# Kernel optimization log

Hardware: AMD Instinct MI355X
Metric: run time of the kernel (lower is better)

Reference implementation:

```python
import jax, jax.numpy as jnp
import numpy as np

N, E, IN, OUT, R, B = 50000, 800000, 16, 16, 90, 30


def setup_inputs() -> dict:
    key = jax.random.key(0)
    ks = jax.random.split(key, 9)
    h = jax.random.normal(ks[0], (N, IN), dtype=jnp.float32)
    he = jax.random.normal(ks[1], (E, IN), dtype=jnp.float32)
    Ws = jax.random.normal(ks[2], (OUT, IN), dtype=jnp.float32) * 0.1      # shared_weight.weight
    Wa = jax.random.normal(ks[3], (1, 3 * OUT), dtype=jnp.float32) * 0.1   # attn_fc.weight
    weight = jax.random.normal(ks[4], (B, IN, OUT), dtype=jnp.float32) * 0.1  # basis weights
    w_comp = jax.random.normal(ks[5], (R, B), dtype=jnp.float32) * 0.1        # basis coefficients
    src = jax.random.randint(ks[6], (E,), 0, N)
    dst = jax.random.randint(ks[7], (E,), 0, N)
    rel_type = jax.random.randint(ks[8], (E,), 0, R)
    return {"h": h, "he": he, "Ws": Ws, "Wa": Wa, "weight": weight,
            "w_comp": w_comp, "src": src, "dst": dst, "rel_type": rel_type}


def reference(h, he, Ws, Wa, weight, w_comp, src, dst, rel_type):
    n_nodes, in_dim = h.shape
    num_bases, _, out_dim = weight.shape
    num_rels = w_comp.shape[0]

    # Basis decomposition, replicating the original's reshape semantics exactly:
    # view [B,in,out] -> [in,B,out], matmul with w_comp [R,B] -> [in,R,out], view -> [R,in,out]
    V = weight.reshape(in_dim, num_bases, out_dim)
    W_rel = jnp.matmul(w_comp, V).reshape(num_rels, in_dim, out_dim)  # [R,in,out]

    # edge_attention: GAT-like score from concat(z_src, z_edge, z_dst)
    h_src = h[src]                      # [E,in]
    z_src = h_src @ Ws.T                # [E,out]
    z_dst = h[dst] @ Ws.T               # [E,out]
    z_e = he @ Ws.T                     # [E,out]
    e = jnp.concatenate([z_src, z_e, z_dst], axis=1) @ Wa.T  # [E,1] (no leaky_relu / no softmax in original)

    # message: per-edge relation-specific bmm, scaled by attention score
    msg = jnp.einsum('ei,eio->eo', h_src, W_rel[rel_type]) * e  # [E,out]

    # reduce: scatter-sum into destination nodes (bias=None, activation=None)
    h_out = jax.ops.segment_sum(msg, dst, num_segments=n_nodes)  # [N,out]
    return h_out
```

## Files before the change

### kernel.cpp

```cpp
#include <hip/hip_runtime.h>

#define N_NODES 50000
#define N_EDGES 800000
#define IN_DIM 16
#define OUT_DIM 16
#define N_RELS 90
#define N_BASES 30

#define CAP 64
#define LDS_STRIDE 260

#define PREP_BLOCKS 91
#define DOTS_BLOCKS 196
#define ZERO_BLOCKS 196
#define HZ_BLOCKS 782

#define NODES_PER_RBLK 256

__device__ __forceinline__ float4 shfl_xor4(float4 v, int m) {
    float4 r;
    r.x = __shfl_xor(v.x, m); r.y = __shfl_xor(v.y, m);
    r.z = __shfl_xor(v.z, m); r.w = __shfl_xor(v.w, m);
    return r;
}

__global__ __launch_bounds__(256) void setup_kernel(
    const float* __restrict__ Ws,
    const float* __restrict__ Wa,
    const float* __restrict__ weight,
    const float* __restrict__ w_comp,
    const float* __restrict__ h,
    float* __restrict__ Wrel,
    float* __restrict__ avec,
    float2* __restrict__ s13,
    int* __restrict__ cnt,
    float* __restrict__ hout)
{
    int b = blockIdx.x;
    if (b < PREP_BLOCKS) {
        int f = b * 256 + threadIdx.x;
        if (f < N_RELS * IN_DIM * OUT_DIM) {
            int a   = f / (N_RELS * OUT_DIM);
            int rem = f % (N_RELS * OUT_DIM);
            int r   = rem / OUT_DIM;
            int o   = rem % OUT_DIM;
            float acc = 0.f;
            #pragma unroll
            for (int bb = 0; bb < N_BASES; ++bb)
                acc += w_comp[r * N_BASES + bb] * weight[a * (N_BASES * OUT_DIM) + bb * OUT_DIM + o];
            Wrel[f] = acc;
        } else if (f < N_RELS * IN_DIM * OUT_DIM + 48) {
            int g = f - N_RELS * IN_DIM * OUT_DIM;
            int k = g / IN_DIM;
            int i = g % IN_DIM;
            float acc = 0.f;
            #pragma unroll
            for (int o = 0; o < OUT_DIM; ++o)
                acc += Wa[k * OUT_DIM + o] * Ws[o * IN_DIM + i];
            avec[g] = acc;
        }
    } else if (b < PREP_BLOCKS + DOTS_BLOCKS) {
        __shared__ float la[48];
        if (threadIdx.x < 48) {
            int k = threadIdx.x / IN_DIM;
            int i = threadIdx.x % IN_DIM;
            float acc = 0.f;
            #pragma unroll
            for (int o = 0; o < OUT_DIM; ++o)
                acc += Wa[k * OUT_DIM + o] * Ws[o * IN_DIM + i];
            la[threadIdx.x] = acc;
        }
        __syncthreads();
        int n = (b - PREP_BLOCKS) * 256 + threadIdx.x;
        if (n >= N_NODES) return;
        const float4* p = (const float4*)(h + (size_t)n * IN_DIM);
        float d1 = 0.f, d3 = 0.f;
        #pragma unroll
        for (int i = 0; i < 4; ++i) {
            float4 v = p[i];
            d1 += v.x * la[4*i+0] + v.y * la[4*i+1] + v.z * la[4*i+2] + v.w * la[4*i+3];
            d3 += v.x * la[32+4*i+0] + v.y * la[32+4*i+1] + v.z * la[32+4*i+2] + v.w * la[32+4*i+3];
        }
        s13[n] = make_float2(d1, d3);
    } else if (b < PREP_BLOCKS + DOTS_BLOCKS + ZERO_BLOCKS) {
        int n = (b - PREP_BLOCKS - DOTS_BLOCKS) * 256 + threadIdx.x;
        if (n < N_NODES) cnt[n] = 0;
    } else {
        int idx = (b - PREP_BLOCKS - DOTS_BLOCKS - ZERO_BLOCKS) * 256 + threadIdx.x;
        if (idx < N_NODES * OUT_DIM / 4) {
            float4 z = {0.f, 0.f, 0.f, 0.f};
            ((float4*)hout)[idx] = z;
        }
    }
}

__global__ __launch_bounds__(256) void route_kernel(
    const float* __restrict__ h,
    const float* __restrict__ he,
    const int* __restrict__ src,
    const int* __restrict__ dst,
    const int* __restrict__ rel,
    const float* __restrict__ Wrel,
    const float* __restrict__ avec,
    const float2* __restrict__ s13,
    int* __restrict__ cnt,
    uint2* __restrict__ bucket,
    float* __restrict__ hout)
{
    int e = blockIdx.x * 256 + threadIdx.x;
    if (e >= N_EDGES) return;
    int s = src[e], d = dst[e], r = rel[e];

    const float4* hep = (const float4*)(he + (size_t)e * IN_DIM);
    const float4* ap  = (const float4*)(avec + 16);
    float pd = 0.f;
    #pragma unroll
    for (int i = 0; i < 4; ++i) {
        float4 v = hep[i];
        float4 a = ap[i];
        pd += v.x * a.x + v.y * a.y + v.z * a.z + v.w * a.w;
    }
    float2 ss = s13[s];
    float2 sd = s13[d];
    float score = ss.x + sd.y + pd;

    int slot = atomicAdd(&cnt[d], 1);
    if (slot < CAP) {
        uint2 ent;
        ent.x = ((unsigned)r << 16) | (unsigned)s;
        ent.y = __float_as_uint(score);
        bucket[(size_t)d * CAP + slot] = ent;
    } else {
        float hs[16];
        const float4* hp = (const float4*)(h + (size_t)s * IN_DIM);
        #pragma unroll
        for (int i = 0; i < 4; ++i) {
            float4 v = hp[i];
            hs[4*i+0] = v.x; hs[4*i+1] = v.y; hs[4*i+2] = v.z; hs[4*i+3] = v.w;
        }
        const float* W = Wrel + (size_t)r * 256;
        float* outp = hout + (size_t)d * OUT_DIM;
        #pragma unroll
        for (int o = 0; o < OUT_DIM; ++o) {
            float acc = 0.f;
            #pragma unroll
            for (int i = 0; i < IN_DIM; ++i) acc += hs[i] * W[i * OUT_DIM + o];
            atomicAdd(outp + o, acc * score);
        }
    }
}

__global__ __launch_bounds__(1024) void reduce_bmm_kernel(
    const float* __restrict__ h,
    const float* __restrict__ Wrel,
    const uint2* __restrict__ bucket,
    const int* __restrict__ cnt,
    float* __restrict__ hout)
{
    extern __shared__ float lw[];
    for (int j = threadIdx.x; j < N_RELS * 64; j += 1024) {
        int r = j >> 6;
        int w = j & 63;
        float4 v = ((const float4*)Wrel)[r * 64 + w];
        *(float4*)(lw + r * LDS_STRIDE + w * 4) = v;
    }
    __syncthreads();

    int n = blockIdx.x * NODES_PER_RBLK + (threadIdx.x >> 2);
    int q = threadIdx.x & 3;
    if (n >= N_NODES) return;

    int deg = cnt[n];
    int m = deg > CAP ? CAP : deg;
    const uint2* ep = bucket + (size_t)n * CAP;
    float4 acc = {0.f, 0.f, 0.f, 0.f};

    for (int j0 = 0; j0 < m; j0 += 4) {
        uint2 ent[4];
        float4 hq[4];
        bool val[4];

        #pragma unroll
        for (int k = 0; k < 4; ++k) {
            int j = j0 + k;
            val[k] = (j < m);
            int jc = j < m ? j : (m - 1);
            ent[k] = ep[jc];
        }

        #pragma unroll
        for (int k = 0; k < 4; ++k) {
            int s = ent[k].x & 0xFFFF;
            hq[k] = *(const float4*)(h + (size_t)s * IN_DIM + q * 4);
        }

        #pragma unroll
        for (int k = 0; k < 4; ++k) {
            if (!val[k]) continue;
            int r = ent[k].x >> 16;
            float score = __uint_as_float(ent[k].y);

            float4 o1 = shfl_xor4(hq[k], 1);
            float4 o2 = shfl_xor4(hq[k], 2);
            float4 o3 = shfl_xor4(o1, 2);
            bool q0 = (q == 0), q1 = (q == 1), q2 = (q == 2);
            float4 row0 = q0 ? hq[k] : q1 ? o1 : q2 ? o2 : o3;
            float4 row1 = q0 ? o1 : q1 ? hq[k] : q2 ? o3 : o2;
            float4 row2 = q0 ? o2 : q1 ? o3 : q2 ? hq[k] : o1;
            float4 row3 = q0 ? o3 : q1 ? o2 : q2 ? o1 : hq[k];
            float hs[16] = {row0.x,row0.y,row0.z,row0.w, row1.x,row1.y,row1.z,row1.w,
                            row2.x,row2.y,row2.z,row2.w, row3.x,row3.y,row3.z,row3.w};

            const float* wb = lw + (size_t)r * LDS_STRIDE + q * 4;
            float4 a = {0.f, 0.f, 0.f, 0.f};
            #pragma unroll
            for (int i = 0; i < 16; ++i) {
                float4 w = *(const float4*)(wb + i * 16);
                float hv = hs[i];
                a.x += hv * w.x; a.y += hv * w.y; a.z += hv * w.z; a.w += hv * w.w;
            }
            acc.x += score * a.x; acc.y += score * a.y;
            acc.z += score * a.z; acc.w += score * a.w;
        }
    }

    float* outp = hout + (size_t)n * OUT_DIM + q * 4;
    if (deg <= CAP) {
        *(float4*)outp = acc;
    } else {
        atomicAdd(outp + 0, acc.x);
        atomicAdd(outp + 1, acc.y);
        atomicAdd(outp + 2, acc.z);
        atomicAdd(outp + 3, acc.w);
    }
}

__global__ __launch_bounds__(256) void prep_kernel(
    const float* __restrict__ Ws, const float* __restrict__ Wa,
    const float* __restrict__ weight, const float* __restrict__ w_comp,
    float* __restrict__ Wrel, float* __restrict__ avec)
{
    int f = blockIdx.x * blockDim.x + threadIdx.x;
    if (f < N_RELS * IN_DIM * OUT_DIM) {
        int a   = f / (N_RELS * OUT_DIM);
        int rem = f % (N_RELS * OUT_DIM);
        int r   = rem / OUT_DIM;
        int o   = rem % OUT_DIM;
        float acc = 0.f;
        #pragma unroll
        for (int b = 0; b < N_BASES; ++b)
            acc += w_comp[r * N_BASES + b] * weight[a * (N_BASES * OUT_DIM) + b * OUT_DIM + o];
        Wrel[f] = acc;
    } else if (f < N_RELS * IN_DIM * OUT_DIM + 48) {
        int g = f - N_RELS * IN_DIM * OUT_DIM;
        int k = g / IN_DIM;
        int i = g % IN_DIM;
        float acc = 0.f;
        #pragma unroll
        for (int o = 0; o < OUT_DIM; ++o)
            acc += Wa[k * OUT_DIM + o] * Ws[o * IN_DIM + i];
        avec[g] = acc;
    }
}

__global__ __launch_bounds__(256) void edge_atomic_kernel(
    const float* __restrict__ h,
    const float* __restrict__ he,
    const int* __restrict__ src,
    const int* __restrict__ dst,
    const int* __restrict__ rel,
    const float* __restrict__ Wrel,
    const float* __restrict__ avec,
    float* __restrict__ hout)
{
    int e = blockIdx.x * blockDim.x + threadIdx.x;
    if (e >= N_EDGES) return;
    int s = src[e], d = dst[e], r = rel[e];
    float hs[IN_DIM];
    const float4* p = (const float4*)(h + (size_t)s * IN_DIM);
    #pragma unroll
    for (int i = 0; i < 4; ++i) {
        float4 v = p[i];
        hs[4*i+0] = v.x; hs[4*i+1] = v.y; hs[4*i+2] = v.z; hs[4*i+3] = v.w;
    }
    float score = 0.f;
    #pragma unroll
    for (int i = 0; i < IN_DIM; ++i) score += hs[i] * avec[i];
    const float4* qe = (const float4*)(he + (size_t)e * IN_DIM);
    #pragma unroll
    for (int i = 0; i < 4; ++i) {
        float4 v = qe[i];
        score += v.x * avec[16+4*i] + v.y * avec[17+4*i] + v.z * avec[18+4*i] + v.w * avec[19+4*i];
    }
    const float4* pd = (const float4*)(h + (size_t)d * IN_DIM);
    #pragma unroll
    for (int i = 0; i < 4; ++i) {
        float4 v = pd[i];
        score += v.x * avec[32+4*i] + v.y * avec[33+4*i] + v.z * avec[34+4*i] + v.w * avec[35+4*i];
    }
    float acc[OUT_DIM];
    #pragma unroll
    for (int o = 0; o < OUT_DIM; ++o) acc[o] = 0.f;
    const float* W = Wrel + (size_t)r * 256;
    #pragma unroll
    for (int i = 0; i < IN_DIM; ++i) {
        float hv = hs[i];
        #pragma unroll
        for (int o = 0; o < OUT_DIM; ++o) acc[o] += hv * W[i * OUT_DIM + o];
    }
    float* outp = hout + (size_t)d * OUT_DIM;
    #pragma unroll
    for (int o = 0; o < OUT_DIM; ++o) atomicAdd(outp + o, acc[o] * score);
}

extern "C" void kernel_launch(void* const* d_in, const int* in_sizes, int n_in,
                              void* d_out, int out_size, void* d_ws, size_t ws_size,
                              hipStream_t stream) {
    const float* h      = (const float*)d_in[0];
    const float* he     = (const float*)d_in[1];
    const float* Ws     = (const float*)d_in[2];
    const float* Wa     = (const float*)d_in[3];
    const float* weight = (const float*)d_in[4];
    const float* w_comp = (const float*)d_in[5];
    const int*   src    = (const int*)d_in[6];
    const int*   dst    = (const int*)d_in[7];
    const int*   rel    = (const int*)d_in[8];
    float* hout = (float*)d_out;

    const size_t OFF_WREL   = 0;
    const size_t OFF_AVEC   = 23040;
    const size_t OFF_S13    = 23104;
    const size_t OFF_CNT    = 123104;
    const size_t OFF_BUCKET = 173104;
    const size_t NEED_BUCKET = OFF_BUCKET * 4 + (size_t)N_NODES * CAP * sizeof(uint2);

    float* wsf  = (float*)d_ws;
    float* Wrel = wsf + OFF_WREL;
    float* avec = wsf + OFF_AVEC;
    float2* s13 = (float2*)(wsf + OFF_S13);
    int* cnt    = (int*)(wsf + OFF_CNT);

    if (ws_size >= NEED_BUCKET) {
        uint2* bucket = (uint2*)(wsf + OFF_BUCKET);

        setup_kernel<<<PREP_BLOCKS + DOTS_BLOCKS + ZERO_BLOCKS + HZ_BLOCKS, 256, 0, stream>>>(
            Ws, Wa, weight, w_comp, h, Wrel, avec, s13, cnt, hout);
        route_kernel<<<N_EDGES / 256, 256, 0, stream>>>(
            h, he, src, dst, rel, Wrel, avec, s13, cnt, bucket, hout);
        reduce_bmm_kernel<<<(N_NODES + NODES_PER_RBLK - 1) / NODES_PER_RBLK, 1024,
                            N_RELS * LDS_STRIDE * sizeof(float), stream>>>(
            h, Wrel, bucket, cnt, hout);
    } else {
        hipMemsetAsync(d_out, 0, (size_t)out_size * sizeof(float), stream);
        int total = N_RELS * IN_DIM * OUT_DIM + 48;
        prep_kernel<<<(total + 255) / 256, 256, 0, stream>>>(Ws, Wa, weight, w_comp, Wrel, avec);
        edge_atomic_kernel<<<(N_EDGES + 255) / 256, 256, 0, stream>>>(
            h, he, src, dst, rel, Wrel, avec, hout);
    }
}
```

Measured before the change: 187.9 us.

## Batch four edges per route thread and split node reduction across 16 lanes

The route kernel now has each thread process four edges, issuing all index, edge-feature and score loads before the atomics so more memory requests are in flight. The reduce kernel assigns 16 lanes per node instead of 4, with four lane groups each handling a strided subset of bucket entries and combining results through warp shuffles. This raises parallelism in the reduce stage (782 blocks instead of 196) at the cost of repeated LDS weight staging per block and extra shuffle reductions. Low-degree nodes leave more lanes idle.

Result: slower. 203.8 us (+8.4%).

```diff
diff --git a/kernel.cpp b/kernel.cpp
--- a/kernel.cpp
+++ b/kernel.cpp
@@ -15,7 +15,9 @@
 #define ZERO_BLOCKS 196
 #define HZ_BLOCKS 782
 
-#define NODES_PER_RBLK 256
+#define ROUTE_BLOCKS 784
+#define RNODES_PER_BLK 64
+#define REDUCE_BLOCKS 782
 
 __device__ __forceinline__ float4 shfl_xor4(float4 v, int m) {
     float4 r;
@@ -107,45 +109,68 @@
     uint2* __restrict__ bucket,
     float* __restrict__ hout)
 {
-    int e = blockIdx.x * 256 + threadIdx.x;
-    if (e >= N_EDGES) return;
-    int s = src[e], d = dst[e], r = rel[e];
-
-    const float4* hep = (const float4*)(he + (size_t)e * IN_DIM);
-    const float4* ap  = (const float4*)(avec + 16);
-    float pd = 0.f;
-    #pragma unroll
-    for (int i = 0; i < 4; ++i) {
-        float4 v = hep[i];
-        float4 a = ap[i];
-        pd += v.x * a.x + v.y * a.y + v.z * a.z + v.w * a.w;
-    }
-    float2 ss = s13[s];
-    float2 sd = s13[d];
-    float score = ss.x + sd.y + pd;
-
-    int slot = atomicAdd(&cnt[d], 1);
-    if (slot < CAP) {
-        uint2 ent;
-        ent.x = ((unsigned)r << 16) | (unsigned)s;
-        ent.y = __float_as_uint(score);
-        bucket[(size_t)d * CAP + slot] = ent;
-    } else {
-        float hs[16];
-        const float4* hp = (const float4*)(h + (size_t)s * IN_DIM);
-        #pragma unroll
-        for (int i = 0; i < 4; ++i) {
-            float4 v = hp[i];
-            hs[4*i+0] = v.x; hs[4*i+1] = v.y; hs[4*i+2] = v.z; hs[4*i+3] = v.w;
-        }
-        const float* W = Wrel + (size_t)r * 256;
-        float* outp = hout + (size_t)d * OUT_DIM;
-        #pragma unroll
-        for (int o = 0; o < OUT_DIM; ++o) {
-            float acc = 0.f;
-            #pragma unroll
-            for (int i = 0; i < IN_DIM; ++i) acc += hs[i] * W[i * OUT_DIM + o];
-            atomicAdd(outp + o, acc * score);
+    const int tid  = threadIdx.x;
+    const int ebeg = blockIdx.x * 1024;
+
+    const float4* ap = (const float4*)(avec + 16);
+    float4 a0 = ap[0], a1 = ap[1], a2 = ap[2], a3 = ap[3];
+
+    int e[4], s[4], d[4], r[4];
+    bool val[4];
+    #pragma unroll
+    for (int c = 0; c < 4; ++c) {
+        e[c] = ebeg + c * 256 + tid;
+        val[c] = (e[c] < N_EDGES);
+        int ec = val[c] ? e[c] : 0;
+        s[c] = src[ec]; d[c] = dst[ec]; r[c] = rel[ec];
+    }
+
+    float pd[4];
+    float2 ss[4], sd[4];
+    #pragma unroll
+    for (int c = 0; c < 4; ++c) {
+        int ec = val[c] ? e[c] : 0;
+        const float4* hep = (const float4*)(he + (size_t)ec * IN_DIM);
+        float4 v0 = hep[0], v1 = hep[1], v2 = hep[2], v3 = hep[3];
+        pd[c] = v0.x*a0.x + v0.y*a0.y + v0.z*a0.z + v0.w*a0.w
+              + v1.x*a1.x + v1.y*a1.y + v1.z*a1.z + v1.w*a1.w
+              + v2.x*a2.x + v2.y*a2.y + v2.z*a2.z + v2.w*a2.w
+              + v3.x*a3.x + v3.y*a3.y + v3.z*a3.z + v3.w*a3.w;
+        ss[c] = s13[s[c]];
+        sd[c] = s13[d[c]];
+    }
+
+    int slot[4];
+    #pragma unroll
+    for (int c = 0; c < 4; ++c)
+        slot[c] = val[c] ? atomicAdd(&cnt[d[c]], 1) : 0;
+
+    #pragma unroll
+    for (int c = 0; c < 4; ++c) {
+        if (!val[c]) continue;
+        float score = ss[c].x + sd[c].y + pd[c];
+        if (slot[c] < CAP) {
+            uint2 ent;
+            ent.x = ((unsigned)r[c] << 16) | (unsigned)s[c];
+            ent.y = __float_as_uint(score);
+            bucket[(size_t)d[c] * CAP + slot[c]] = ent;
+        } else {
+            float hs[16];
+            const float4* hp = (const float4*)(h + (size_t)s[c] * IN_DIM);
+            #pragma unroll
+            for (int i = 0; i < 4; ++i) {
+                float4 v = hp[i];
+                hs[4*i+0] = v.x; hs[4*i+1] = v.y; hs[4*i+2] = v.z; hs[4*i+3] = v.w;
+            }
+            const float* W = Wrel + (size_t)r[c] * 256;
+            float* outp = hout + (size_t)d[c] * OUT_DIM;
+            #pragma unroll
+            for (int o = 0; o < OUT_DIM; ++o) {
+                float acc = 0.f;
+                #pragma unroll
+                for (int i = 0; i < IN_DIM; ++i) acc += hs[i] * W[i * OUT_DIM + o];
+                atomicAdd(outp + o, acc * score);
+            }
         }
     }
 }
@@ -166,8 +191,10 @@
     }
     __syncthreads();
 
-    int n = blockIdx.x * NODES_PER_RBLK + (threadIdx.x >> 2);
-    int q = threadIdx.x & 3;
+    int n = blockIdx.x * RNODES_PER_BLK + (threadIdx.x >> 4);
+    int l = threadIdx.x & 15;
+    int q = l & 3;
+    int p = l >> 2;
     if (n >= N_NODES) return;
 
     int deg = cnt[n];
@@ -175,27 +202,26 @@
     const uint2* ep = bucket + (size_t)n * CAP;
     float4 acc = {0.f, 0.f, 0.f, 0.f};
 
-    for (int j0 = 0; j0 < m; j0 += 4) {
-        uint2 ent[4];
-        float4 hq[4];
-        bool val[4];
-
-        #pragma unroll
-        for (int k = 0; k < 4; ++k) {
-            int j = j0 + k;
+    for (int j0 = 0; j0 < m; j0 += 8) {
+        uint2 ent[2];
+        float4 hq[2];
+        bool val[2];
+
+        #pragma unroll
+        for (int k = 0; k < 2; ++k) {
+            int j = j0 + p * 2 + k;
             val[k] = (j < m);
-            int jc = j < m ? j : (m - 1);
-            ent[k] = ep[jc];
-        }
-
-        #pragma unroll
-        for (int k = 0; k < 4; ++k) {
-            int s = ent[k].x & 0xFFFF;
-            hq[k] = *(const float4*)(h + (size_t)s * IN_DIM + q * 4);
-        }
-
-        #pragma unroll
-        for (int k = 0; k < 4; ++k) {
+            ent[k] = ep[val[k] ? j : 0];
+        }
+
+        #pragma unroll
+        for (int k = 0; k < 2; ++k) {
+            int sidx = ent[k].x & 0xFFFF;
+            hq[k] = *(const float4*)(h + (size_t)sidx * IN_DIM + q * 4);
+        }
+
+        #pragma unroll
+        for (int k = 0; k < 2; ++k) {
             if (!val[k]) continue;
             int r = ent[k].x >> 16;
             float score = __uint_as_float(ent[k].y);
@@ -224,14 +250,21 @@
         }
     }
 
-    float* outp = hout + (size_t)n * OUT_DIM + q * 4;
-    if (deg <= CAP) {
-        *(float4*)outp = acc;
-    } else {
-        atomicAdd(outp + 0, acc.x);
-        atomicAdd(outp + 1, acc.y);
-        atomicAdd(outp + 2, acc.z);
-        atomicAdd(outp + 3, acc.w);
+    acc.x += __shfl_xor(acc.x, 4); acc.y += __shfl_xor(acc.y, 4);
+    acc.z += __shfl_xor(acc.z, 4); acc.w += __shfl_xor(acc.w, 4);
+    acc.x += __shfl_xor(acc.x, 8); acc.y += __shfl_xor(acc.y, 8);
+    acc.z += __shfl_xor(acc.z, 8); acc.w += __shfl_xor(acc.w, 8);
+
+    if (p == 0) {
+        float* outp = hout + (size_t)n * OUT_DIM + q * 4;
+        if (deg <= CAP) {
+            *(float4*)outp = acc;
+        } else {
+            atomicAdd(outp + 0, acc.x);
+            atomicAdd(outp + 1, acc.y);
+            atomicAdd(outp + 2, acc.z);
+            atomicAdd(outp + 3, acc.w);
+        }
     }
 }
 
@@ -345,9 +378,9 @@
 
         setup_kernel<<<PREP_BLOCKS + DOTS_BLOCKS + ZERO_BLOCKS + HZ_BLOCKS, 256, 0, stream>>>(
             Ws, Wa, weight, w_comp, h, Wrel, avec, s13, cnt, hout);
-        route_kernel<<<N_EDGES / 256, 256, 0, stream>>>(
+        route_kernel<<<ROUTE_BLOCKS, 256, 0, stream>>>(
             h, he, src, dst, rel, Wrel, avec, s13, cnt, bucket, hout);
-        reduce_bmm_kernel<<<(N_NODES + NODES_PER_RBLK - 1) / NODES_PER_RBLK, 1024,
+        reduce_bmm_kernel<<<REDUCE_BLOCKS, 1024,
                             N_RELS * LDS_STRIDE * sizeof(float), stream>>>(
             h, Wrel, bucket, cnt, hout);
     } else {
```

## Split per-node reduce across 16 lanes and defer score node terms to reduce

Applied to the files above, without the earlier changes.

The reduce kernel now gives each destination node 16 lanes instead of 4, with four groups each taking two edges per step and combining partial sums through cross-lane shuffles. The intent is more parallelism and memory-level concurrency on the gather for the low-degree nodes. The route kernel no longer reads s13 for the source and destination of bucketed edges and stores only the edge-feature part of the score. The reduce adds the source and destination terms itself, which moves those random reads into the kernel that already gathers h[src]. The cost is an extra s13 read per edge in the reduce, shuffle reductions, and 4x more reduce blocks, each of which reloads the relation-weight tables into LDS.

Result: slower. 193.3 us (+2.9%).

```diff
diff --git a/kernel.cpp b/kernel.cpp
--- a/kernel.cpp
+++ b/kernel.cpp
@@ -15,7 +15,9 @@
 #define ZERO_BLOCKS 196
 #define HZ_BLOCKS 782
 
-#define NODES_PER_RBLK 256
+#define ROUTE_BLOCKS 3125
+#define RNODES_PER_BLK 64
+#define REDUCE_BLOCKS 782
 
 __device__ __forceinline__ float4 shfl_xor4(float4 v, int m) {
     float4 r;
@@ -120,17 +122,17 @@
         float4 a = ap[i];
         pd += v.x * a.x + v.y * a.y + v.z * a.z + v.w * a.w;
     }
-    float2 ss = s13[s];
-    float2 sd = s13[d];
-    float score = ss.x + sd.y + pd;
 
     int slot = atomicAdd(&cnt[d], 1);
     if (slot < CAP) {
         uint2 ent;
         ent.x = ((unsigned)r << 16) | (unsigned)s;
-        ent.y = __float_as_uint(score);
+        ent.y = __float_as_uint(pd);
         bucket[(size_t)d * CAP + slot] = ent;
     } else {
+        float2 ss = s13[s];
+        float2 sd = s13[d];
+        float score = ss.x + sd.y + pd;
         float hs[16];
         const float4* hp = (const float4*)(h + (size_t)s * IN_DIM);
         #pragma unroll
@@ -153,6 +155,7 @@
 __global__ __launch_bounds__(1024) void reduce_bmm_kernel(
     const float* __restrict__ h,
     const float* __restrict__ Wrel,
+    const float2* __restrict__ s13,
     const uint2* __restrict__ bucket,
     const int* __restrict__ cnt,
     float* __restrict__ hout)
@@ -166,39 +169,43 @@
     }
     __syncthreads();
 
-    int n = blockIdx.x * NODES_PER_RBLK + (threadIdx.x >> 2);
-    int q = threadIdx.x & 3;
+    int n = blockIdx.x * RNODES_PER_BLK + (threadIdx.x >> 4);
+    int l = threadIdx.x & 15;
+    int q = l & 3;
+    int p = l >> 2;
     if (n >= N_NODES) return;
 
     int deg = cnt[n];
     int m = deg > CAP ? CAP : deg;
     const uint2* ep = bucket + (size_t)n * CAP;
+    float s3n = s13[n].y;
     float4 acc = {0.f, 0.f, 0.f, 0.f};
 
-    for (int j0 = 0; j0 < m; j0 += 4) {
-        uint2 ent[4];
-        float4 hq[4];
-        bool val[4];
-
-        #pragma unroll
-        for (int k = 0; k < 4; ++k) {
-            int j = j0 + k;
+    for (int j0 = 0; j0 < m; j0 += 8) {
+        uint2 ent[2];
+        float4 hq[2];
+        float s1v[2];
+        bool val[2];
+
+        #pragma unroll
+        for (int k = 0; k < 2; ++k) {
+            int j = j0 + p * 2 + k;
             val[k] = (j < m);
-            int jc = j < m ? j : (m - 1);
-            ent[k] = ep[jc];
-        }
-
-        #pragma unroll
-        for (int k = 0; k < 4; ++k) {
-            int s = ent[k].x & 0xFFFF;
-            hq[k] = *(const float4*)(h + (size_t)s * IN_DIM + q * 4);
-        }
-
-        #pragma unroll
-        for (int k = 0; k < 4; ++k) {
+            ent[k] = ep[val[k] ? j : 0];
+        }
+
+        #pragma unroll
+        for (int k = 0; k < 2; ++k) {
+            int sidx = ent[k].x & 0xFFFF;
+            hq[k]  = *(const float4*)(h + (size_t)sidx * IN_DIM + q * 4);
+            s1v[k] = s13[sidx].x;
+        }
+
+        #pragma unroll
+        for (int k = 0; k < 2; ++k) {
             if (!val[k]) continue;
             int r = ent[k].x >> 16;
-            float score = __uint_as_float(ent[k].y);
+            float score = s1v[k] + s3n + __uint_as_float(ent[k].y);
 
             float4 o1 = shfl_xor4(hq[k], 1);
             float4 o2 = shfl_xor4(hq[k], 2);
@@ -224,14 +231,21 @@
         }
     }
 
-    float* outp = hout + (size_t)n * OUT_DIM + q * 4;
-    if (deg <= CAP) {
-        *(float4*)outp = acc;
-    } else {
-        atomicAdd(outp + 0, acc.x);
-        atomicAdd(outp + 1, acc.y);
-        atomicAdd(outp + 2, acc.z);
-        atomicAdd(outp + 3, acc.w);
+    acc.x += __shfl_xor(acc.x, 4); acc.y += __shfl_xor(acc.y, 4);
+    acc.z += __shfl_xor(acc.z, 4); acc.w += __shfl_xor(acc.w, 4);
+    acc.x += __shfl_xor(acc.x, 8); acc.y += __shfl_xor(acc.y, 8);
+    acc.z += __shfl_xor(acc.z, 8); acc.w += __shfl_xor(acc.w, 8);
+
+    if (p == 0) {
+        float* outp = hout + (size_t)n * OUT_DIM + q * 4;
+        if (deg <= CAP) {
+            *(float4*)outp = acc;
+        } else {
+            atomicAdd(outp + 0, acc.x);
+            atomicAdd(outp + 1, acc.y);
+            atomicAdd(outp + 2, acc.z);
+            atomicAdd(outp + 3, acc.w);
+        }
     }
 }
 
@@ -345,11 +359,11 @@
 
         setup_kernel<<<PREP_BLOCKS + DOTS_BLOCKS + ZERO_BLOCKS + HZ_BLOCKS, 256, 0, stream>>>(
             Ws, Wa, weight, w_comp, h, Wrel, avec, s13, cnt, hout);
-        route_kernel<<<N_EDGES / 256, 256, 0, stream>>>(
+        route_kernel<<<ROUTE_BLOCKS, 256, 0, stream>>>(
             h, he, src, dst, rel, Wrel, avec, s13, cnt, bucket, hout);
-        reduce_bmm_kernel<<<(N_NODES + NODES_PER_RBLK - 1) / NODES_PER_RBLK, 1024,
+        reduce_bmm_kernel<<<REDUCE_BLOCKS, 1024,
                             N_RELS * LDS_STRIDE * sizeof(float), stream>>>(
-            h, Wrel, bucket, cnt, hout);
+            h, Wrel, s13, bucket, cnt, hout);
     } else {
         hipMemsetAsync(d_out, 0, (size_t)out_size * sizeof(float), stream);
         int total = N_RELS * IN_DIM * OUT_DIM + 48;
```
